# Optimization experiments

Measured on AMD Instinct MI355X. Metric: run time of the kernel, lower is better.

The kernel has to match this reference:

```python
import jax, jax.numpy as jnp
import numpy as np

N, IN_DIM, HID, ENC = 2048, 128, 64, 64
B, SEQ = 64, 12
BN_EPS = 1e-5


def setup_inputs() -> dict:
    key = jax.random.key(0)
    ks = jax.random.split(key, 20)
    glorot = lambda k, shape: jax.random.uniform(k, shape, jnp.float32,
                                                 -jnp.sqrt(6.0 / (shape[0] + shape[1])),
                                                 jnp.sqrt(6.0 / (shape[0] + shape[1])))
    return {
        'h': jax.random.normal(ks[0], (N, IN_DIM), jnp.float32),
        'adj': jax.random.uniform(ks[1], (N, N), jnp.float32),
        'inputs': jax.random.normal(ks[2], (B, SEQ, N), jnp.float32),
        # Extractor_N2V params
        'ew1': glorot(ks[3], (HID, IN_DIM)), 'eb1': jnp.zeros((HID,), jnp.float32),
        'ew2': glorot(ks[4], (ENC, HID)), 'eb2': jnp.zeros((ENC,), jnp.float32),
        'eps1': jnp.ones((1,), jnp.float32),
        'bnw': jnp.ones((ENC,), jnp.float32), 'bnb': jnp.zeros((ENC,), jnp.float32),
        # VGRUCell params
        'w1': glorot(ks[5], (HID + 1, 2 * HID)), 'b1': jnp.ones((2 * HID,), jnp.float32),
        'w2': glorot(ks[6], (HID + 1, HID)), 'b2': jnp.zeros((HID,), jnp.float32),
        'wg': glorot(ks[7], (ENC, ENC)), 'bg': jnp.zeros((1,), jnp.float32),
        'wl_w': glorot(ks[8], (HID, HID + ENC)), 'wl_b': jnp.zeros((HID,), jnp.float32),
    }


def _extractor(h, adj, ew1, eb1, ew2, eb2, eps1, bnw, bnb):
    x = h @ ew1.T + eb1                                  # [N, HID]
    pooled = adj @ x                                     # GIN spmm aggregation
    deg = jnp.sum(adj, axis=1, keepdims=True)            # adj @ ones
    deg = jnp.where(deg < 1e-6, 1.0, deg)
    x = pooled / deg + eps1 * x                          # eps-weighted residual combine
    mean = jnp.mean(x, axis=0)
    var = jnp.var(x, axis=0)                             # biased var (torch BN training)
    x = (x - mean) * jax.lax.rsqrt(var + BN_EPS) * bnw + bnb
    return x @ ew2.T + eb2                               # [N, ENC]


def _vgru_linear(x_t, hs, w, b, out_dim):
    # x_t: [B, N], hs: [B, N*HID] -> [B, N*out_dim]
    cc = jnp.concatenate([x_t[..., None], hs.reshape(B, N, HID)], axis=2)
    return (cc.reshape(B * N, HID + 1) @ w + b).reshape(B, N * out_dim)


def reference(h, adj, inputs, ew1, eb1, ew2, eb2, eps1, bnw, bnb,
              w1, b1, w2, b2, wg, bg, wl_w, wl_b):
    feat = _extractor(h, adj, ew1, eb1, ew2, eb2, eps1, bnw, bnb)   # [N, ENC]
    feat_p = jnp.broadcast_to(feat, (B, N, ENC)).reshape(B * N, ENC) @ wg + bg

    def step(hs, x_t):
        ru = jax.nn.sigmoid(_vgru_linear(x_t, hs, w1, b1, 2 * HID))  # [B, N*2H]
        r, u = jnp.split(ru, 2, axis=1)                              # chunk dim=1
        c = jnp.tanh(_vgru_linear(x_t, r * hs, w2, b2, HID))
        new = u * hs + (1.0 - u) * c
        nh = new.reshape(B * N, HID)
        nh = jnp.concatenate([nh, feat_p], axis=1)                   # need_road=True
        nh = (nh @ wl_w.T + wl_b).reshape(B, N * HID)
        return nh, None

    hs0 = jnp.zeros((B, N * HID), inputs.dtype)
    hs_final, _ = jax.lax.scan(step, hs0, jnp.swapaxes(inputs, 0, 1))  # [SEQ,B,N]
    return hs_final.reshape(B * N, HID)
```

## Files before the change

### kernel.cpp

```cpp
#include <hip/hip_runtime.h>
#include <cstdint>


typedef _Float16 half8 __attribute__((ext_vector_type(8)));
typedef _Float16 half4 __attribute__((ext_vector_type(4)));
typedef float f32x4 __attribute__((ext_vector_type(4)));

static __device__ inline f32x4 mfma16(half8 a, half8 b, f32x4 c) {
  return __builtin_amdgcn_mfma_f32_16x16x32_f16(a, b, c, 0, 0, 0);
}

static __device__ inline float fast_sigmoid(float x) {
  return __builtin_amdgcn_rcpf(1.f + __expf(-x));
}
static __device__ inline float fast_tanh(float x) {
  return 1.f - 2.f * __builtin_amdgcn_rcpf(__expf(2.f * x) + 1.f);
}

static __device__ inline int afr4(int n, int k) {
  return ((n >> 4) * 2 + (k >> 5)) * 512 +
         (((n & 15) | (((k >> 3) & 3) << 4)) * 8) + (k & 7);
}

static __device__ inline int hso4(int n, int k) {
  return n * 64 + (((k >> 3) ^ ((n >> 1) & 7)) * 8) + (k & 7);
}

__global__ __launch_bounds__(256) void extract1(
    const float* __restrict__ h, const float* __restrict__ ew1,
    const float* __restrict__ eb1, float* __restrict__ x1,
    _Float16* __restrict__ x1f)
{
  int idx = blockIdx.x * 256 + threadIdx.x;
  int n = idx >> 6, j = idx & 63;
  const float4* hr = (const float4*)(h + (size_t)n * 128);
  const float4* wr = (const float4*)(ew1 + (size_t)j * 128);
  float acc = eb1[j];
#pragma unroll
  for (int k4 = 0; k4 < 32; ++k4) {
    float4 a = hr[k4], w = wr[k4];
    acc += a.x * w.x + a.y * w.y + a.z * w.z + a.w * w.w;
  }
  x1[idx] = acc;
  int ks = n >> 5, nt = j >> 4;
  int l = (j & 15) | (((n >> 3) & 3) << 4);
  x1f[(((ks * 4 + nt) * 64) + l) * 8 + (n & 7)] = (_Float16)acc;
}

__global__ __launch_bounds__(256) void extract2_mfma(
    const float* __restrict__ adj, const float* __restrict__ x1,
    const _Float16* __restrict__ x1f, const float* __restrict__ eps1,
    float* __restrict__ x2)
{
  const int n0 = blockIdx.x * 8;
  const int t = threadIdx.x;
  const int l = t & 63, wv = t >> 6;
  __shared__ __align__(16) _Float16 Abuf[4096];
  __shared__ float deg_l[8];

  for (int i = t; i < 4096; i += 256) Abuf[i] = (_Float16)0.f;

  const int row = t >> 5;
  const int kcol = (t & 31) * 8;
  const int s_my = (t & 31) >> 2;
  const int c_my = t & 3;

  float degp = 0.f;
  f32x4 acc = {0.f, 0.f, 0.f, 0.f};

  for (int kc = 0; kc < 8; ++kc) {
    __syncthreads();
    {
      const float* src = &adj[(size_t)(n0 + row) * 2048 + kc * 256 + kcol];
      float4 p0 = *(const float4*)src;
      float4 p1 = *(const float4*)(src + 4);
      degp += p0.x + p0.y + p0.z + p0.w + p1.x + p1.y + p1.z + p1.w;
      half8 v;
      v[0] = (_Float16)p0.x; v[1] = (_Float16)p0.y;
      v[2] = (_Float16)p0.z; v[3] = (_Float16)p0.w;
      v[4] = (_Float16)p1.x; v[5] = (_Float16)p1.y;
      v[6] = (_Float16)p1.z; v[7] = (_Float16)p1.w;
      *(half8*)&Abuf[(size_t)(s_my * 64 + (row | (c_my << 4))) * 8] = v;
    }
    __syncthreads();
#pragma unroll
    for (int s = 0; s < 8; ++s) {
      half8 A = *(half8*)&Abuf[(s * 64 + l) * 8];
      half8 B = *(const half8*)&x1f[(size_t)(((kc * 8 + s) * 4 + wv) * 64 + l) * 8];
      acc = mfma16(A, B, acc);
    }
  }

  for (int sh = 16; sh >= 1; sh >>= 1) degp += __shfl_down(degp, sh, 32);
  if ((t & 31) == 0) deg_l[row] = degp;
  __syncthreads();

  const float ep = eps1[0];
  int colc = wv * 16 + (l & 15);
  int r0 = (l >> 4) * 4;
  if (r0 < 8) {
#pragma unroll
    for (int q = 0; q < 4; ++q) {
      int r = r0 + q;
      float d = deg_l[r];
      d = (d < 1e-6f) ? 1.f : d;
      size_t off = (size_t)(n0 + r) * 64 + colc;
      x2[off] = acc[q] / d + ep * x1[off];
    }
  }
}

__global__ __launch_bounds__(256) void extract3a(
    const float* __restrict__ x2, float* __restrict__ psum,
    float* __restrict__ pqsum)
{
  int g = blockIdx.x;
  int t = threadIdx.x, j = t & 63, rg = t >> 6;
  __shared__ float sl[4][64], ql[4][64];
  float s = 0.f, q = 0.f;
  for (int r = g * 32 + rg; r < g * 32 + 32; r += 4) {
    float v = x2[(size_t)r * 64 + j];
    s += v; q += v * v;
  }
  sl[rg][j] = s; ql[rg][j] = q;
  __syncthreads();
  if (t < 64) {
    psum[g * 64 + t]  = sl[0][t] + sl[1][t] + sl[2][t] + sl[3][t];
    pqsum[g * 64 + t] = ql[0][t] + ql[1][t] + ql[2][t] + ql[3][t];
  }
}

__global__ void extract3b(
    const float* __restrict__ psum, const float* __restrict__ pqsum,
    const float* __restrict__ bnw, const float* __restrict__ bnb,
    float* __restrict__ scale, float* __restrict__ shift)
{
  int j = threadIdx.x;
  float s = 0.f, q = 0.f;
  for (int g = 0; g < 64; ++g) { s += psum[g * 64 + j]; q += pqsum[g * 64 + j]; }
  float mean = s * (1.f / 2048.f);
  float var = q * (1.f / 2048.f) - mean * mean;
  float rstd = rsqrtf(var + 1e-5f);
  float sc = rstd * bnw[j];
  scale[j] = sc;
  shift[j] = bnb[j] - mean * sc;
}

__global__ __launch_bounds__(256) void extract4(
    const float* __restrict__ x2, const float* __restrict__ scale,
    const float* __restrict__ shift, const float* __restrict__ ew2,
    const float* __restrict__ eb2, const float* __restrict__ wg,
    const float* __restrict__ bg, const float* __restrict__ wl_w,
    const float* __restrict__ wl_b, _Float16* __restrict__ fplC)
{
  __shared__ float xn[4][64], ft[4][64], fp[4][64];
  int t = threadIdx.x, sub = t >> 6, o = t & 63;
  int n = blockIdx.x * 4 + sub;
  xn[sub][o] = x2[(size_t)n * 64 + o] * scale[o] + shift[o];
  __syncthreads();
  {
    float acc = eb2[o];
    for (int k = 0; k < 64; ++k) acc += xn[sub][k] * ew2[o * 64 + k];
    ft[sub][o] = acc;
  }
  __syncthreads();
  {
    float acc = bg[0];
    for (int k = 0; k < 64; ++k) acc += ft[sub][k] * wg[k * 64 + o];
    fp[sub][o] = acc;
  }
  __syncthreads();
  {
    float acc = wl_b[o];
    for (int k = 0; k < 64; ++k) acc += fp[sub][k] * wl_w[o * 128 + 64 + k];
    int tile = n >> 6;
    int ntp = (n >> 4) & 3;
    int lane = (n & 15) | (((o >> 2) & 3) << 4);
    fplC[(((tile * 4 + (o >> 4)) * 256) + ntp * 64 + lane) * 4 + (o & 3)] =
        (_Float16)acc;
  }
}

__global__ __launch_bounds__(256) void prep_frags(
    const float* __restrict__ w1, const float* __restrict__ w2,
    const float* __restrict__ wl_w, _Float16* __restrict__ w1f,
    _Float16* __restrict__ w2f, _Float16* __restrict__ wlf)
{
  int idx = blockIdx.x * 256 + threadIdx.x;
  int e = idx & 7, l = (idx >> 3) & 63;
  int kk = ((l >> 4) * 8) + e;
  if (idx < 8192) {
    int ks = (idx >> 9) & 1, nt = idx >> 10;
    int k = ks * 32 + kk;
    w1f[idx] = (_Float16)w1[(1 + k) * 128 + nt * 16 + (l & 15)];
  } else if (idx < 12288) {
    int i2 = idx - 8192;
    int ks = (i2 >> 9) & 1, nt = i2 >> 10;
    int k = ks * 32 + kk;
    w2f[i2] = (_Float16)w2[(1 + k) * 64 + nt * 16 + (l & 15)];
  } else {
    int i3 = idx - 12288;
    int ks = (i3 >> 9) & 1, nt = i3 >> 10;
    int k = ks * 32 + kk;
    wlf[i3] = (_Float16)wl_w[(nt * 16 + (l & 15)) * 128 + k];
  }
}

__global__ __launch_bounds__(256, 4) void gru_step(
    const _Float16* __restrict__ hs_in, void* __restrict__ hs_out_v,
    int outF32, const float* __restrict__ inputs, int tstep, int first,
    const float* __restrict__ w1, const float* __restrict__ b1,
    const float* __restrict__ w2, const float* __restrict__ b2,
    const _Float16* __restrict__ fplC, const _Float16* __restrict__ w1f,
    const _Float16* __restrict__ w2f, const _Float16* __restrict__ wlf)
{
  const int tile = blockIdx.x;
  const int bA   = blockIdx.y;
  const int a = tile * 64;
  const int t = threadIdx.x;
  const int l = t & 63, wv = t >> 6;
  const int lq = l >> 4, li = l & 15;
  const int halfBase = a >> 1;

  __shared__ __align__(16) _Float16 Asrc[4096];
  __shared__ __align__(16) _Float16 A2f[4096];
  __shared__ __align__(16) _Float16 uF[4096];
  __shared__ __align__(16) _Float16 hsOwn[4096];
  __shared__ float xts[64], xto[64];

  half8 Aw1[2][2];
#pragma unroll
  for (int q = 0; q < 2; ++q)
#pragma unroll
    for (int ks = 0; ks < 2; ++ks)
      Aw1[q][ks] = *(const half8*)&w1f[((((2 * wv + q) * 2 + ks) * 64) + l) * 8];
  half8 Aw2[2], Awl[2];
#pragma unroll
  for (int ks = 0; ks < 2; ++ks) {
    Aw2[ks] = *(const half8*)&w2f[(((wv * 2 + ks) * 64) + l) * 8];
    Awl[ks] = *(const half8*)&wlf[(((wv * 2 + ks) * 64) + l) * 8];
  }
  half4 fpl4[4];
#pragma unroll
  for (int nt = 0; nt < 4; ++nt)
    fpl4[nt] = *(const half4*)&fplC[(((tile * 4 + wv) * 256) + nt * 64 + l) * 4];
  float bjR[2][4], w1xR[2][4];
#pragma unroll
  for (int q = 0; q < 2; ++q)
#pragma unroll
    for (int qq = 0; qq < 4; ++qq) {
      int j = (2 * wv + q) * 16 + lq * 4 + qq;
      bjR[q][qq] = b1[j];
      w1xR[q][qq] = w1[j];
    }
  float b2R[4], w2xR[4];
#pragma unroll
  for (int qq = 0; qq < 4; ++qq) {
    int o = wv * 16 + lq * 4 + qq;
    b2R[qq] = b2[o];
    w2xR[qq] = w2[o];
  }
  const int bit = wv >> 1;

  for (int uu = 0; uu < 2; ++uu) {
    const int b = bA + uu * 32;
    const float* xt = inputs + (size_t)(b * 12 + tstep) * 2048;
    const _Float16* hsb = hs_in + (size_t)b * 131072;

    __syncthreads();

    if (t < 64) {
      xto[t] = xt[a + t];
    } else if (t < 128) {
      int m = t - 64;
      int ns = (m < 32) ? (halfBase + m) : (1024 + halfBase + m - 32);
      xts[m] = xt[ns];
    }
    for (int i = t; i < 512; i += 256) {
      int m = i >> 3, k8 = i & 7;
      half8 v, vo;
      if (first) {
#pragma unroll
        for (int e = 0; e < 8; ++e) v[e] = (_Float16)0.f;
        vo = v;
      } else {
        int ns = (m < 32) ? (halfBase + m) : (1024 + halfBase + m - 32);
        v  = *(const half8*)&hsb[(size_t)ns * 64 + k8 * 8];
        vo = *(const half8*)&hsb[(size_t)(a + m) * 64 + k8 * 8];
      }
      int mt = m >> 4, ks = k8 >> 2, kc = k8 & 3;
      *(half8*)&Asrc[(((mt * 2 + ks) * 64) + ((m & 15) | (kc << 4))) * 8] = v;
      *(half8*)&hsOwn[m * 64 + ((k8 ^ ((m >> 1) & 7)) * 8)] = vo;
    }
    __syncthreads();

    float xtsR[4], xtoR[4];
#pragma unroll
    for (int nt = 0; nt < 4; ++nt) {
      xtsR[nt] = xts[nt * 16 + li];
      xtoR[nt] = xto[nt * 16 + li];
    }

#pragma unroll
    for (int nt = 0; nt < 4; ++nt) {
      half8 Ba = *(half8*)&Asrc[(((nt * 2 + 0) * 64) + l) * 8];
      half8 Bb = *(half8*)&Asrc[(((nt * 2 + 1) * 64) + l) * 8];
      const int n = 2 * ((nt & 1) * 16 + li) + bit;
#pragma unroll
      for (int q = 0; q < 2; ++q) {
        f32x4 acc;
#pragma unroll
        for (int qq = 0; qq < 4; ++qq)
          acc[qq] = bjR[q][qq] + xtsR[nt] * w1xR[q][qq];
        acc = mfma16(Aw1[q][0], Ba, acc);
        acc = mfma16(Aw1[q][1], Bb, acc);
        const int jt = 2 * wv + q;
        const int k0 = (jt & 3) * 16 + lq * 4;
        half4 g4;
#pragma unroll
        for (int qq = 0; qq < 4; ++qq)
          g4[qq] = (_Float16)fast_sigmoid(acc[qq]);
        const int fa = afr4(n, k0);
        if (nt < 2) {
          half4 hv = *(half4*)&hsOwn[hso4(n, k0)];
          half4 r4 = g4 * hv;
          *(half4*)&A2f[fa] = r4;
        } else {
          *(half4*)&uF[fa] = g4;
        }
      }
    }
    __syncthreads();

#pragma unroll
    for (int nt = 0; nt < 4; ++nt) {
      half8 Ba = *(half8*)&A2f[(((nt * 2 + 0) * 64) + l) * 8];
      half8 Bb = *(half8*)&A2f[(((nt * 2 + 1) * 64) + l) * 8];
      f32x4 acc;
#pragma unroll
      for (int qq = 0; qq < 4; ++qq)
        acc[qq] = b2R[qq] + xtoR[nt] * w2xR[qq];
      acc = mfma16(Aw2[0], Ba, acc);
      acc = mfma16(Aw2[1], Bb, acc);
      const int n = nt * 16 + li;
      const int o0 = wv * 16 + lq * 4;
      half4 c4;
#pragma unroll
      for (int qq = 0; qq < 4; ++qq)
        c4[qq] = (_Float16)fast_tanh(acc[qq]);
      const int fa = afr4(n, o0);
      half4 uv = *(half4*)&uF[fa];
      half4 hv = *(half4*)&hsOwn[hso4(n, o0)];
      half4 one = {(_Float16)1.f, (_Float16)1.f, (_Float16)1.f, (_Float16)1.f};
      half4 nw = uv * hv + (one - uv) * c4;
      *(half4*)&Asrc[fa] = nw;
    }
    __syncthreads();

#pragma unroll
    for (int nt = 0; nt < 4; ++nt) {
      half8 Ba = *(half8*)&Asrc[(((nt * 2 + 0) * 64) + l) * 8];
      half8 Bb = *(half8*)&Asrc[(((nt * 2 + 1) * 64) + l) * 8];
      f32x4 acc;
#pragma unroll
      for (int qq = 0; qq < 4; ++qq)
        acc[qq] = (float)fpl4[nt][qq];
      acc = mfma16(Awl[0], Ba, acc);
      acc = mfma16(Awl[1], Bb, acc);
      const int n = nt * 16 + li;
      const int o0 = wv * 16 + lq * 4;
      const size_t base = (size_t)b * 131072 + (size_t)(a + n) * 64 + o0;
      if (outF32) {
        float4 o4 = make_float4(acc[0], acc[1], acc[2], acc[3]);
        *(float4*)&((float*)hs_out_v)[base] = o4;
      } else {
        half4 o4;
#pragma unroll
        for (int qq = 0; qq < 4; ++qq) o4[qq] = (_Float16)acc[qq];
        *(half4*)&((_Float16*)hs_out_v)[base] = o4;
      }
    }
  }
}

extern "C" void kernel_launch(void* const* d_in, const int* in_sizes, int n_in,
                              void* d_out, int out_size, void* d_ws, size_t ws_size,
                              hipStream_t stream) {
  const float* h      = (const float*)d_in[0];
  const float* adj    = (const float*)d_in[1];
  const float* inputs = (const float*)d_in[2];
  const float* ew1    = (const float*)d_in[3];
  const float* eb1    = (const float*)d_in[4];
  const float* ew2    = (const float*)d_in[5];
  const float* eb2    = (const float*)d_in[6];
  const float* eps1   = (const float*)d_in[7];
  const float* bnw    = (const float*)d_in[8];
  const float* bnb    = (const float*)d_in[9];
  const float* w1     = (const float*)d_in[10];
  const float* b1     = (const float*)d_in[11];
  const float* w2     = (const float*)d_in[12];
  const float* b2     = (const float*)d_in[13];
  const float* wg     = (const float*)d_in[14];
  const float* bg     = (const float*)d_in[15];
  const float* wl_w   = (const float*)d_in[16];
  const float* wl_b   = (const float*)d_in[17];

  char* ws = (char*)d_ws;

  _Float16* h0H = (_Float16*)ws;
  _Float16* h1H = (_Float16*)(ws + 16777216);
  float* x1    = (float*)h1H;
  float* x2    = x1 + 131072;
  _Float16* x1f = (_Float16*)(x2 + 131072);
  float* psum  = (float*)(x1f + 131072);
  float* pqsum = psum + 4096;
  float* scale = pqsum + 4096;
  float* shift = scale + 64;
  _Float16* fplC = (_Float16*)(ws + 33554432);
  _Float16* w1f  = fplC + 131072;
  _Float16* w2f  = w1f + 8192;
  _Float16* wlf  = w2f + 4096;

  extract1<<<512, 256, 0, stream>>>(h, ew1, eb1, x1, x1f);
  extract2_mfma<<<256, 256, 0, stream>>>(adj, x1, x1f, eps1, x2);
  extract3a<<<64, 256, 0, stream>>>(x2, psum, pqsum);
  extract3b<<<1, 64, 0, stream>>>(psum, pqsum, bnw, bnb, scale, shift);
  extract4<<<512, 256, 0, stream>>>(x2, scale, shift, ew2, eb2, wg, bg,
                                    wl_w, wl_b, fplC);
  prep_frags<<<64, 256, 0, stream>>>(w1, w2, wl_w, w1f, w2f, wlf);

  dim3 grid(32, 32);
  for (int t = 0; t < 12; ++t) {
    const _Float16* ibuf = (t & 1) ? h0H : h1H;
    void* obuf; int of32 = 0;
    if (t == 11) { obuf = d_out; of32 = 1; }
    else obuf = (t & 1) ? (void*)h1H : (void*)h0H;
    gru_step<<<grid, 256, 0, stream>>>(ibuf, obuf, of32, inputs, t,
                                       (t == 0) ? 1 : 0,
                                       w1, b1, w2, b2, fplC, w1f, w2f, wlf);
  }
}
```

Before: 251.1 us.

## Fuse extractor kernels, atomic BN stats, and prefetch next batch hidden state

The weight-fragment prep is merged into the first extractor kernel. BatchNorm sum and sum-of-squares are now accumulated with atomics inside the aggregation kernel, and scale/shift are computed at the start of the final extractor kernel. Together these cut the pre-GRU launches from six to three. In the GRU step kernel, hidden-state loads for the second batch are issued into registers before the first batch is computed, so global latency overlaps with compute. Costs are extra register pressure and non-deterministic float atomics in the BN statistics.

```diff
diff --git a/kernel.cpp b/kernel.cpp
--- a/kernel.cpp
+++ b/kernel.cpp
@@ -26,31 +26,58 @@
   return n * 64 + (((k >> 3) ^ ((n >> 1) & 7)) * 8) + (k & 7);
 }
 
-__global__ __launch_bounds__(256) void extract1(
+__global__ __launch_bounds__(256) void extract1p(
     const float* __restrict__ h, const float* __restrict__ ew1,
-    const float* __restrict__ eb1, float* __restrict__ x1,
-    _Float16* __restrict__ x1f)
+    const float* __restrict__ eb1, const float* __restrict__ w1,
+    const float* __restrict__ w2, const float* __restrict__ wl_w,
+    float* __restrict__ x1, _Float16* __restrict__ x1f,
+    _Float16* __restrict__ w1f, _Float16* __restrict__ w2f,
+    _Float16* __restrict__ wlf, float* __restrict__ psums)
 {
-  int idx = blockIdx.x * 256 + threadIdx.x;
-  int n = idx >> 6, j = idx & 63;
-  const float4* hr = (const float4*)(h + (size_t)n * 128);
-  const float4* wr = (const float4*)(ew1 + (size_t)j * 128);
-  float acc = eb1[j];
-#pragma unroll
-  for (int k4 = 0; k4 < 32; ++k4) {
-    float4 a = hr[k4], w = wr[k4];
-    acc += a.x * w.x + a.y * w.y + a.z * w.z + a.w * w.w;
-  }
-  x1[idx] = acc;
-  int ks = n >> 5, nt = j >> 4;
-  int l = (j & 15) | (((n >> 3) & 3) << 4);
-  x1f[(((ks * 4 + nt) * 64) + l) * 8 + (n & 7)] = (_Float16)acc;
-}
-
-__global__ __launch_bounds__(256) void extract2_mfma(
+  const int bx = blockIdx.x, t = threadIdx.x;
+  if (bx < 512) {
+    int idx = bx * 256 + t;
+    int n = idx >> 6, j = idx & 63;
+    const float4* hr = (const float4*)(h + (size_t)n * 128);
+    const float4* wr = (const float4*)(ew1 + (size_t)j * 128);
+    float acc = eb1[j];
+#pragma unroll
+    for (int k4 = 0; k4 < 32; ++k4) {
+      float4 a = hr[k4], w = wr[k4];
+      acc += a.x * w.x + a.y * w.y + a.z * w.z + a.w * w.w;
+    }
+    x1[idx] = acc;
+    int ks = n >> 5, nt = j >> 4;
+    int l = (j & 15) | (((n >> 3) & 3) << 4);
+    x1f[(((ks * 4 + nt) * 64) + l) * 8 + (n & 7)] = (_Float16)acc;
+  } else {
+    if (bx == 512 && t < 128) psums[t] = 0.f;
+    int idx = (bx - 512) * 256 + t;
+    int e = idx & 7, l = (idx >> 3) & 63;
+    int kk = ((l >> 4) * 8) + e;
+    if (idx < 8192) {
+      int ks = (idx >> 9) & 1, nt = idx >> 10;
+      int k = ks * 32 + kk;
+      w1f[idx] = (_Float16)w1[(1 + k) * 128 + nt * 16 + (l & 15)];
+    } else if (idx < 12288) {
+      int i2 = idx - 8192;
+      int ks = (i2 >> 9) & 1, nt = i2 >> 10;
+      int k = ks * 32 + kk;
+      w2f[i2] = (_Float16)w2[(1 + k) * 64 + nt * 16 + (l & 15)];
+    } else {
+      int i3 = idx - 12288;
+      int ks = (i3 >> 9) & 1, nt = i3 >> 10;
+      int k = ks * 32 + kk;
+      wlf[i3] = (_Float16)wl_w[(nt * 16 + (l & 15)) * 128 + k];
+    }
+  }
+}
+
+__global__ __launch_bounds__(256) void extract2s(
     const float* __restrict__ adj, const float* __restrict__ x1,
     const _Float16* __restrict__ x1f, const float* __restrict__ eps1,
-    float* __restrict__ x2)
+    float* __restrict__ x2, float* __restrict__ psum,
+    float* __restrict__ pqsum)
 {
   const int n0 = blockIdx.x * 8;
   const int t = threadIdx.x;
@@ -96,8 +123,9 @@
   __syncthreads();
 
   const float ep = eps1[0];
-  int colc = wv * 16 + (l & 15);
-  int r0 = (l >> 4) * 4;
+  const int colc = wv * 16 + (l & 15);
+  const int r0 = (l >> 4) * 4;
+  float ps = 0.f, qs = 0.f;
   if (r0 < 8) {
 #pragma unroll
     for (int q = 0; q < 4; ++q) {
@@ -105,58 +133,42 @@
       float d = deg_l[r];
       d = (d < 1e-6f) ? 1.f : d;
       size_t off = (size_t)(n0 + r) * 64 + colc;
-      x2[off] = acc[q] / d + ep * x1[off];
-    }
-  }
-}
-
-__global__ __launch_bounds__(256) void extract3a(
-    const float* __restrict__ x2, float* __restrict__ psum,
-    float* __restrict__ pqsum)
-{
-  int g = blockIdx.x;
-  int t = threadIdx.x, j = t & 63, rg = t >> 6;
-  __shared__ float sl[4][64], ql[4][64];
-  float s = 0.f, q = 0.f;
-  for (int r = g * 32 + rg; r < g * 32 + 32; r += 4) {
-    float v = x2[(size_t)r * 64 + j];
-    s += v; q += v * v;
-  }
-  sl[rg][j] = s; ql[rg][j] = q;
-  __syncthreads();
-  if (t < 64) {
-    psum[g * 64 + t]  = sl[0][t] + sl[1][t] + sl[2][t] + sl[3][t];
-    pqsum[g * 64 + t] = ql[0][t] + ql[1][t] + ql[2][t] + ql[3][t];
-  }
-}
-
-__global__ void extract3b(
-    const float* __restrict__ psum, const float* __restrict__ pqsum,
-    const float* __restrict__ bnw, const float* __restrict__ bnb,
-    float* __restrict__ scale, float* __restrict__ shift)
-{
-  int j = threadIdx.x;
-  float s = 0.f, q = 0.f;
-  for (int g = 0; g < 64; ++g) { s += psum[g * 64 + j]; q += pqsum[g * 64 + j]; }
-  float mean = s * (1.f / 2048.f);
-  float var = q * (1.f / 2048.f) - mean * mean;
-  float rstd = rsqrtf(var + 1e-5f);
-  float sc = rstd * bnw[j];
-  scale[j] = sc;
-  shift[j] = bnb[j] - mean * sc;
-}
-
-__global__ __launch_bounds__(256) void extract4(
-    const float* __restrict__ x2, const float* __restrict__ scale,
-    const float* __restrict__ shift, const float* __restrict__ ew2,
+      float xv = acc[q] / d + ep * x1[off];
+      x2[off] = xv;
+      ps += xv; qs += xv * xv;
+    }
+  }
+  ps += __shfl_down(ps, 16, 64);
+  qs += __shfl_down(qs, 16, 64);
+  if ((l >> 4) == 0) {
+    atomicAdd(&psum[colc], ps);
+    atomicAdd(&pqsum[colc], qs);
+  }
+}
+
+__global__ __launch_bounds__(256) void extract4s(
+    const float* __restrict__ x2, const float* __restrict__ psum,
+    const float* __restrict__ pqsum, const float* __restrict__ bnw,
+    const float* __restrict__ bnb, const float* __restrict__ ew2,
     const float* __restrict__ eb2, const float* __restrict__ wg,
     const float* __restrict__ bg, const float* __restrict__ wl_w,
     const float* __restrict__ wl_b, _Float16* __restrict__ fplC)
 {
   __shared__ float xn[4][64], ft[4][64], fp[4][64];
+  __shared__ float scl[64], shf[64];
   int t = threadIdx.x, sub = t >> 6, o = t & 63;
   int n = blockIdx.x * 4 + sub;
-  xn[sub][o] = x2[(size_t)n * 64 + o] * scale[o] + shift[o];
+  if (t < 64) {
+    float s = psum[t], q = pqsum[t];
+    float mean = s * (1.f / 2048.f);
+    float var = q * (1.f / 2048.f) - mean * mean;
+    float rstd = rsqrtf(var + 1e-5f);
+    float sc = rstd * bnw[t];
+    scl[t] = sc;
+    shf[t] = bnb[t] - mean * sc;
+  }
+  __syncthreads();
+  xn[sub][o] = x2[(size_t)n * 64 + o] * scl[o] + shf[o];
   __syncthreads();
   {
     float acc = eb2[o];
@@ -178,31 +190,6 @@
     int lane = (n & 15) | (((o >> 2) & 3) << 4);
     fplC[(((tile * 4 + (o >> 4)) * 256) + ntp * 64 + lane) * 4 + (o & 3)] =
         (_Float16)acc;
-  }
-}
-
-__global__ __launch_bounds__(256) void prep_frags(
-    const float* __restrict__ w1, const float* __restrict__ w2,
-    const float* __restrict__ wl_w, _Float16* __restrict__ w1f,
-    _Float16* __restrict__ w2f, _Float16* __restrict__ wlf)
-{
-  int idx = blockIdx.x * 256 + threadIdx.x;
-  int e = idx & 7, l = (idx >> 3) & 63;
-  int kk = ((l >> 4) * 8) + e;
-  if (idx < 8192) {
-    int ks = (idx >> 9) & 1, nt = idx >> 10;
-    int k = ks * 32 + kk;
-    w1f[idx] = (_Float16)w1[(1 + k) * 128 + nt * 16 + (l & 15)];
-  } else if (idx < 12288) {
-    int i2 = idx - 8192;
-    int ks = (i2 >> 9) & 1, nt = i2 >> 10;
-    int k = ks * 32 + kk;
-    w2f[i2] = (_Float16)w2[(1 + k) * 64 + nt * 16 + (l & 15)];
-  } else {
-    int i3 = idx - 12288;
-    int ks = (i3 >> 9) & 1, nt = i3 >> 10;
-    int k = ks * 32 + kk;
-    wlf[i3] = (_Float16)wl_w[(nt * 16 + (l & 15)) * 128 + k];
   }
 }
 
@@ -262,13 +249,40 @@
   }
   const int bit = wv >> 1;
 
+  const int m0 = t >> 3, k80 = t & 7;
+  const int m1 = (t + 256) >> 3, k81 = t & 7;
+  const int ns0 = (m0 < 32) ? (halfBase + m0) : (1024 + halfBase + m0 - 32);
+  const int ns1 = (m1 < 32) ? (halfBase + m1) : (1024 + halfBase + m1 - 32);
+
+  half8 pv[2], pvo[2];
+  {
+    const _Float16* hsb = hs_in + (size_t)(bA) * 131072;
+    if (first) {
+#pragma unroll
+      for (int e = 0; e < 8; ++e) { pv[0][e] = (_Float16)0.f; }
+      pv[1] = pv[0]; pvo[0] = pv[0]; pvo[1] = pv[0];
+    } else {
+      pv[0]  = *(const half8*)&hsb[(size_t)ns0 * 64 + k80 * 8];
+      pvo[0] = *(const half8*)&hsb[(size_t)(a + m0) * 64 + k80 * 8];
+      pv[1]  = *(const half8*)&hsb[(size_t)ns1 * 64 + k81 * 8];
+      pvo[1] = *(const half8*)&hsb[(size_t)(a + m1) * 64 + k81 * 8];
+    }
+  }
+
   for (int uu = 0; uu < 2; ++uu) {
     const int b = bA + uu * 32;
     const float* xt = inputs + (size_t)(b * 12 + tstep) * 2048;
-    const _Float16* hsb = hs_in + (size_t)b * 131072;
-
-    __syncthreads();
-
+
+    __syncthreads();
+
+    {
+      int mt = m0 >> 4, ks = k80 >> 2, kc = k80 & 3;
+      *(half8*)&Asrc[(((mt * 2 + ks) * 64) + ((m0 & 15) | (kc << 4))) * 8] = pv[0];
+      *(half8*)&hsOwn[m0 * 64 + ((k80 ^ ((m0 >> 1) & 7)) * 8)] = pvo[0];
+      mt = m1 >> 4; ks = k81 >> 2; kc = k81 & 3;
+      *(half8*)&Asrc[(((mt * 2 + ks) * 64) + ((m1 & 15) | (kc << 4))) * 8] = pv[1];
+      *(half8*)&hsOwn[m1 * 64 + ((k81 ^ ((m1 >> 1) & 7)) * 8)] = pvo[1];
+    }
     if (t < 64) {
       xto[t] = xt[a + t];
     } else if (t < 128) {
@@ -276,21 +290,12 @@
       int ns = (m < 32) ? (halfBase + m) : (1024 + halfBase + m - 32);
       xts[m] = xt[ns];
     }
-    for (int i = t; i < 512; i += 256) {
-      int m = i >> 3, k8 = i & 7;
-      half8 v, vo;
-      if (first) {
-#pragma unroll
-        for (int e = 0; e < 8; ++e) v[e] = (_Float16)0.f;
-        vo = v;
-      } else {
-        int ns = (m < 32) ? (halfBase + m) : (1024 + halfBase + m - 32);
-        v  = *(const half8*)&hsb[(size_t)ns * 64 + k8 * 8];
-        vo = *(const half8*)&hsb[(size_t)(a + m) * 64 + k8 * 8];
-      }
-      int mt = m >> 4, ks = k8 >> 2, kc = k8 & 3;
-      *(half8*)&Asrc[(((mt * 2 + ks) * 64) + ((m & 15) | (kc << 4))) * 8] = v;
-      *(half8*)&hsOwn[m * 64 + ((k8 ^ ((m >> 1) & 7)) * 8)] = vo;
+    if (uu == 0 && !first) {
+      const _Float16* hsb1 = hs_in + (size_t)(bA + 32) * 131072;
+      pv[0]  = *(const half8*)&hsb1[(size_t)ns0 * 64 + k80 * 8];
+      pvo[0] = *(const half8*)&hsb1[(size_t)(a + m0) * 64 + k80 * 8];
+      pv[1]  = *(const half8*)&hsb1[(size_t)ns1 * 64 + k81 * 8];
+      pvo[1] = *(const half8*)&hsb1[(size_t)(a + m1) * 64 + k81 * 8];
     }
     __syncthreads();
 
@@ -413,21 +418,17 @@
   float* x2    = x1 + 131072;
   _Float16* x1f = (_Float16*)(x2 + 131072);
   float* psum  = (float*)(x1f + 131072);
-  float* pqsum = psum + 4096;
-  float* scale = pqsum + 4096;
-  float* shift = scale + 64;
+  float* pqsum = psum + 64;
   _Float16* fplC = (_Float16*)(ws + 33554432);
   _Float16* w1f  = fplC + 131072;
   _Float16* w2f  = w1f + 8192;
   _Float16* wlf  = w2f + 4096;
 
-  extract1<<<512, 256, 0, stream>>>(h, ew1, eb1, x1, x1f);
-  extract2_mfma<<<256, 256, 0, stream>>>(adj, x1, x1f, eps1, x2);
-  extract3a<<<64, 256, 0, stream>>>(x2, psum, pqsum);
-  extract3b<<<1, 64, 0, stream>>>(psum, pqsum, bnw, bnb, scale, shift);
-  extract4<<<512, 256, 0, stream>>>(x2, scale, shift, ew2, eb2, wg, bg,
-                                    wl_w, wl_b, fplC);
-  prep_frags<<<64, 256, 0, stream>>>(w1, w2, wl_w, w1f, w2f, wlf);
+  extract1p<<<576, 256, 0, stream>>>(h, ew1, eb1, w1, w2, wl_w,
+                                     x1, x1f, w1f, w2f, wlf, psum);
+  extract2s<<<256, 256, 0, stream>>>(adj, x1, x1f, eps1, x2, psum, pqsum);
+  extract4s<<<512, 256, 0, stream>>>(x2, psum, pqsum, bnw, bnb, ew2, eb2,
+                                     wg, bg, wl_w, wl_b, fplC);
 
   dim3 grid(32, 32);
   for (int t = 0; t < 12; ++t) {
```

Result: slower. 268.9 us (+7.1%).
